# Optimization experiments

Measured on AMD Instinct MI355X. Metric: run time of the kernel, lower is better.

The kernel has to match this reference:

```python
import jax, jax.numpy as jnp
import numpy as np
from jax import lax

A = 3          # anchors per scale
C = 80         # num foreground classes (COCO)
NMS_THRESH = 0.45
NMS_TOPK = 400
POST_NMS = 100


def setup_inputs() -> dict:
    key = jax.random.key(0)
    k0, k1, k2 = jax.random.split(key, 3)
    B = 8
    ch = A * (C + 5)  # 255
    # raw head outputs (pre-decode conv activations), modest scale so exp() stays sane
    tip0 = jax.random.normal(k0, (B, ch, 19, 19), jnp.float32) * 0.5
    tip1 = jax.random.normal(k1, (B, ch, 38, 38), jnp.float32) * 0.5
    tip2 = jax.random.normal(k2, (B, ch, 76, 76), jnp.float32) * 0.5
    # standard YOLOv3 COCO anchors, deepest scale (stride 32) first
    anchors0 = jnp.array([[116., 90.], [156., 198.], [373., 326.]], jnp.float32)
    anchors1 = jnp.array([[30., 61.], [62., 45.], [59., 119.]], jnp.float32)
    anchors2 = jnp.array([[10., 13.], [16., 30.], [33., 23.]], jnp.float32)
    return dict(tip0=tip0, tip1=tip1, tip2=tip2,
                anchors0=anchors0, anchors1=anchors1, anchors2=anchors2)


def _decode(tip, anchors, stride):
    """YOLOOutputV3 inference decode. tip: (B, A*(C+5), H, W)."""
    B, _, H, W = tip.shape
    # (B, A*(C+5), H*W) -> (B, H*W, A, C+5)
    pred = tip.reshape(B, A * (C + 5), H * W).transpose(0, 2, 1).reshape(B, H * W, A, C + 5)
    gx, gy = jnp.meshgrid(jnp.arange(W), jnp.arange(H))       # each (H, W)
    offsets = jnp.stack([gx, gy], -1).reshape(1, H * W, 1, 2).astype(tip.dtype)
    centers = (jax.nn.sigmoid(pred[..., :2]) + offsets) * stride          # (B,HW,A,2)
    scales = jnp.exp(pred[..., 2:4]) * anchors.reshape(1, 1, A, 2)        # (B,HW,A,2)
    conf = jax.nn.sigmoid(pred[..., 4:5])                                 # objectness
    cls_scores = jax.nn.sigmoid(pred[..., 5:]) * conf                      # (B,HW,A,C)
    wh = scales * 0.5
    bbox = jnp.concatenate([centers - wh, centers + wh], -1)               # corner format
    return bbox.reshape(B, H * W * A, 4), cls_scores.reshape(B, H * W * A, C)


def _pairwise_iou(b):
    """b: (K,4) corner boxes -> (K,K) IoU."""
    x1, y1, x2, y2 = b[:, 0], b[:, 1], b[:, 2], b[:, 3]
    area = jnp.maximum(x2 - x1, 0.) * jnp.maximum(y2 - y1, 0.)
    iw = jnp.maximum(jnp.minimum(x2[:, None], x2[None, :]) - jnp.maximum(x1[:, None], x1[None, :]), 0.)
    ih = jnp.maximum(jnp.minimum(y2[:, None], y2[None, :]) - jnp.maximum(y1[:, None], y1[None, :]), 0.)
    inter = iw * ih
    return inter / (area[:, None] + area[None, :] - inter + 1e-12)


def _nms_single(det):
    """Class-aware greedy NMS on one image. det: (M,6) = (cid, score, x1,y1,x2,y2)."""
    K = NMS_TOPK
    _, idx = lax.top_k(det[:, 1], K)     # sort by score, keep top K
    d = det[idx]                          # (K,6), descending score
    iou = _pairwise_iou(d[:, 2:6])
    same = d[:, 0][:, None] == d[:, 0][None, :]   # only same class suppresses
    valid = d[:, 1] > 0.
    rng = jnp.arange(K)

    def body(i, keep):
        sup = (iou[i] > NMS_THRESH) & same[i] & (rng > i) & keep[i] & valid[i]
        return keep & ~sup

    keep = lax.fori_loop(0, K, body, jnp.ones((K,), bool)) & valid
    d = jnp.where(keep[:, None], d, jnp.full_like(d, -1.))
    order = jnp.argsort(-d[:, 1])         # kept (sorted) first, suppressed (-1) last
    return d[order][:POST_NMS]            # (POST_NMS, 6)


def _detect(tip0, tip1, tip2, anchors0, anchors1, anchors2):
    dets = []
    for tip, anc, stride in ((tip0, anchors0, 32), (tip1, anchors1, 16), (tip2, anchors2, 8)):
        bbox, scores = _decode(tip, anc, stride)          # (B,N,4), (B,N,C)
        B, N, _ = bbox.shape
        ids = jnp.broadcast_to(jnp.arange(C, dtype=bbox.dtype)[None, None, :, None], (B, N, C, 1))
        sc = scores[..., None]                            # (B,N,C,1)
        bx = jnp.broadcast_to(bbox[:, :, None, :], (B, N, C, 4))
        dets.append(jnp.concatenate([ids, sc, bx], -1).reshape(B, N * C, 6))
    det = jnp.concatenate(dets, 1)                        # (B, M, 6)
    return jax.vmap(_nms_single)(det)                     # (B, POST_NMS, 6)


def reference(tip0, tip1, tip2, anchors0, anchors1, anchors2):
    res = _detect(tip0, tip1, tip2, anchors0, anchors1, anchors2)
    ids = res[..., 0:1]
    scores = res[..., 1:2]
    bboxes = res[..., 2:6]
    return ids, scores, bboxes
```

## Files before the change

### kernel.cpp

```cpp
#include <hip/hip_runtime.h>
#include <stdint.h>

#define NUMA 3
#define NUMC 80
#define CAP  49152
#define CAP2 8192
#define KTOP 400
#define POST 100
#define NBIN1 2048
#define EQCAP 1024
#define KEY0 0x3EE66666u
#define LBUF 1024
#define NMASK (KTOP * 7)

typedef float f32x4 __attribute__((ext_vector_type(4)));

__device__ __forceinline__ float sigmoidf_(float x) { return 1.0f / (1.0f + expf(-x)); }
__device__ __forceinline__ unsigned uminu(unsigned a, unsigned b) { return a < b ? a : b; }

__global__ void init_kernel(unsigned* __restrict__ p) {
    int i = blockIdx.x * blockDim.x + threadIdx.x;
    if (i < NBIN1 * 16 + 40) p[i] = 0;
}

__global__ __launch_bounds__(256) void score_main(
        const float* __restrict__ t0, const float* __restrict__ t1,
        const float* __restrict__ t2,
        unsigned* __restrict__ ccnt, unsigned* __restrict__ ckey,
        unsigned* __restrict__ cidx)
{
    __shared__ unsigned lkey[LBUF], lidx[LBUF];
    __shared__ unsigned lcnt, lbase;
    const int tid = threadIdx.x;
    if (tid == 0) lcnt = 0;
    __syncthreads();

    const int ba = blockIdx.z;
    const int b = ba / 3, a = ba - 3 * b;
    const int c0 = blockIdx.y * 8;
    const int cx = blockIdx.x;

    #define LEMIT(SC, IDX) do { \
        unsigned key_ = __float_as_uint(SC); \
        if (key_ >= KEY0) { \
            unsigned pos_ = atomicAdd(&lcnt, 1u); \
            if (pos_ < LBUF) { lkey[pos_] = key_; lidx[pos_] = (IDX); } \
        } \
    } while (0)

    if (cx < 2) {
        const int hw = cx * 256 + tid;
        if (hw < 361) {
            const float* base = t0 + (size_t)(b * 255 + a * 85) * 361;
            float cr = base[4 * 361 + hw];
            const float* p0 = base + (size_t)(5 + c0) * 361 + hw;
            float x0 = p0[0 * 361], x1 = p0[1 * 361], x2 = p0[2 * 361], x3 = p0[3 * 361];
            float x4 = p0[4 * 361], x5 = p0[5 * 361], x6 = p0[6 * 361], x7 = p0[7 * 361];
            float cf = sigmoidf_(cr);
            unsigned ib = (unsigned)((hw * NUMA + a) * NUMC + c0);
            LEMIT(sigmoidf_(x0) * cf, ib + 0);
            LEMIT(sigmoidf_(x1) * cf, ib + 1);
            LEMIT(sigmoidf_(x2) * cf, ib + 2);
            LEMIT(sigmoidf_(x3) * cf, ib + 3);
            LEMIT(sigmoidf_(x4) * cf, ib + 4);
            LEMIT(sigmoidf_(x5) * cf, ib + 5);
            LEMIT(sigmoidf_(x6) * cf, ib + 6);
            LEMIT(sigmoidf_(x7) * cf, ib + 7);
        }
    } else {
        const float* tip; int vHW, v, candOff;
        if (cx < 4) { tip = t1; vHW = 361;  v = (cx - 2) * 256 + tid; candOff = 86640; }
        else        { tip = t2; vHW = 1444; v = (cx - 4) * 256 + tid; candOff = 433200; }
        if (v < vHW) {
            const f32x4* bp = (const f32x4*)(tip + (size_t)(b * 255 + a * 85) * (size_t)(vHW * 4));
            f32x4 cv = bp[(size_t)4 * vHW + v];
            const f32x4* p0 = bp + (size_t)(5 + c0) * vHW + v;
            f32x4 s0 = p0[0 * (size_t)vHW], s1 = p0[1 * (size_t)vHW];
            f32x4 s2 = p0[2 * (size_t)vHW], s3 = p0[3 * (size_t)vHW];
            f32x4 s4 = p0[4 * (size_t)vHW], s5 = p0[5 * (size_t)vHW];
            f32x4 s6 = p0[6 * (size_t)vHW], s7 = p0[7 * (size_t)vHW];
            float cf0 = sigmoidf_(cv[0]), cf1 = sigmoidf_(cv[1]);
            float cf2 = sigmoidf_(cv[2]), cf3 = sigmoidf_(cv[3]);
            unsigned ib0 = (unsigned)(candOff + (v * 4 * NUMA + a) * NUMC + c0);
            #define EMIT4(S, U) do { \
                unsigned ib = ib0 + (U); \
                LEMIT(sigmoidf_((S)[0]) * cf0, ib); \
                LEMIT(sigmoidf_((S)[1]) * cf1, ib + 240); \
                LEMIT(sigmoidf_((S)[2]) * cf2, ib + 480); \
                LEMIT(sigmoidf_((S)[3]) * cf3, ib + 720); \
            } while (0)
            EMIT4(s0, 0); EMIT4(s1, 1); EMIT4(s2, 2); EMIT4(s3, 3);
            EMIT4(s4, 4); EMIT4(s5, 5); EMIT4(s6, 6); EMIT4(s7, 7);
            #undef EMIT4
        }
    }
    #undef LEMIT

    __syncthreads();
    if (tid == 0) {
        unsigned c = lcnt;
        if (c > LBUF) {
            atomicOr(&ccnt[b], 0x80000000u);
            lbase = 0xFFFFFFFFu;
        } else {
            lbase = atomicAdd(&ccnt[b], c);
        }
    }
    __syncthreads();
    unsigned c = uminu(lcnt, (unsigned)LBUF);
    unsigned basep = lbase;
    if (basep != 0xFFFFFFFFu) {
        for (unsigned i = tid; i < c; i += 256) {
            unsigned p = basep + i;
            if (p < CAP) {
                ckey[(size_t)b * CAP + p] = lkey[i];
                cidx[(size_t)b * CAP + p] = lidx[i];
            }
        }
    }
}

__device__ __forceinline__ void wave_select(const unsigned* h, int nbins, unsigned rank,
                                            unsigned* resv, int tid)
{
    if (tid >= 64) return;
    const int lane = tid;
    const int cs = nbins >> 6;
    unsigned v = 0;
    for (int k = 0; k < cs; k++) {
        int off = (k + lane) & (cs - 1);
        v += h[lane * cs + off];
    }
    unsigned S = v;
    #pragma unroll
    for (int o = 1; o < 64; o <<= 1) {
        unsigned t = (unsigned)__shfl_down((int)S, o);
        if (lane + o < 64) S += t;
    }
    unsigned long long bm = __ballot(S >= rank);
    if (bm == 0ull) bm = 1ull;
    int C = 63 - __builtin_clzll(bm);
    unsigned SC = (unsigned)__builtin_amdgcn_readlane((int)S, C);
    unsigned vC = (unsigned)__builtin_amdgcn_readlane((int)v, C);
    unsigned rem = rank - (SC - vC);
    unsigned w = (lane < cs) ? h[C * cs + lane] : 0u;
    unsigned T = w;
    #pragma unroll
    for (int o = 1; o < 64; o <<= 1) {
        unsigned t = (unsigned)__shfl_down((int)T, o);
        if (lane + o < 64) T += t;
    }
    unsigned long long bm2 = __ballot((T >= rem) && (lane < cs));
    if (bm2 == 0ull) bm2 = 1ull;
    int B = 63 - __builtin_clzll(bm2);
    unsigned TB = (unsigned)__builtin_amdgcn_readlane((int)T, B);
    unsigned wB = (unsigned)__builtin_amdgcn_readlane((int)w, B);
    if (lane == 0) {
        resv[0] = (unsigned)(C * cs + B);
        resv[1] = rem - (TB - wB);
    }
}

__global__ __launch_bounds__(1024) void findcut_v(const unsigned* __restrict__ ckey,
                                                  unsigned* __restrict__ cutfloor,
                                                  unsigned* __restrict__ ccnt,
                                                  unsigned* __restrict__ flags) {
    __shared__ unsigned h[NBIN1];
    __shared__ unsigned resv[2];
    int b = blockIdx.x;
    int tid = threadIdx.x;
    for (int i = tid; i < NBIN1; i += 1024) h[i] = 0;
    unsigned c = ccnt[b];
    bool ok = (c >= KTOP) && (c <= CAP);
    __syncthreads();
    if (ok) {
        const unsigned* ck = ckey + (size_t)b * CAP;
        for (unsigned i = tid; i < c; i += 1024) {
            unsigned bin = (ck[i] - KEY0) >> 13;
            atomicAdd(&h[uminu(bin, NBIN1 - 1)], 1u);
        }
    }
    __syncthreads();
    wave_select(h, NBIN1, KTOP, resv, tid);
    __syncthreads();
    if (tid == 0) {
        flags[b] = ok ? 1u : 0u;
        if (ok) {
            cutfloor[b] = KEY0 + (resv[0] << 13);
        } else {
            cutfloor[b] = 0u;
            ccnt[b] = 0;
        }
    }
}

__global__ __launch_bounds__(256) void fb_hist(
        const float* __restrict__ t0, const float* __restrict__ t1,
        const float* __restrict__ t2,
        unsigned* __restrict__ histF, const unsigned* __restrict__ flags)
{
    const int ba = blockIdx.z;
    const int b = ba / 3, a = ba - 3 * b;
    if (flags[b]) return;
    __shared__ unsigned lh[NBIN1];
    const int tid = threadIdx.x;
    for (int i = tid; i < NBIN1; i += 256) lh[i] = 0;
    __syncthreads();
    const int c0 = blockIdx.y * 8;
    const int cx = blockIdx.x;
    if (cx < 2) {
        const int hw = cx * 256 + tid;
        if (hw < 361) {
            const float* base = t0 + (size_t)(b * 255 + a * 85) * 361;
            float cf = sigmoidf_(base[4 * 361 + hw]);
            for (int u = 0; u < 8; u++) {
                float sc = sigmoidf_(base[(size_t)(5 + c0 + u) * 361 + hw]) * cf;
                atomicAdd(&lh[__float_as_uint(sc) >> 19], 1u);
            }
        }
    } else {
        const float* tip; int vHW, v;
        if (cx < 4) { tip = t1; vHW = 361;  v = (cx - 2) * 256 + tid; }
        else        { tip = t2; vHW = 1444; v = (cx - 4) * 256 + tid; }
        if (v < vHW) {
            const f32x4* bp = (const f32x4*)(tip + (size_t)(b * 255 + a * 85) * (size_t)(vHW * 4));
            f32x4 cv = bp[(size_t)4 * vHW + v];
            float cf[4] = { sigmoidf_(cv[0]), sigmoidf_(cv[1]), sigmoidf_(cv[2]), sigmoidf_(cv[3]) };
            for (int u = 0; u < 8; u++) {
                f32x4 s = bp[(size_t)(5 + c0 + u) * vHW + v];
                for (int l = 0; l < 4; l++)
                    atomicAdd(&lh[__float_as_uint(sigmoidf_(s[l]) * cf[l]) >> 19], 1u);
            }
        }
    }
    __syncthreads();
    unsigned* gh = histF + b * NBIN1;
    for (int i = tid; i < NBIN1; i += 256) {
        unsigned v2 = lh[i];
        if (v2) atomicAdd(&gh[i], v2);
    }
}

__global__ __launch_bounds__(256) void fb_cut(const unsigned* __restrict__ histF,
                                              unsigned* __restrict__ cutb,
                                              const unsigned* __restrict__ flags) {
    int b = blockIdx.x;
    if (flags[b]) return;
    __shared__ unsigned h[NBIN1];
    __shared__ unsigned resv[2];
    for (int i = threadIdx.x; i < NBIN1; i += 256) h[i] = histF[b * NBIN1 + i];
    __syncthreads();
    wave_select(h, NBIN1, KTOP, resv, threadIdx.x);
    __syncthreads();
    if (threadIdx.x == 0) cutb[b] = resv[0];
}

__global__ __launch_bounds__(256) void fb_compact(
        const float* __restrict__ t0, const float* __restrict__ t1,
        const float* __restrict__ t2,
        const unsigned* __restrict__ cutb, unsigned* __restrict__ ccnt,
        unsigned* __restrict__ ckey, unsigned* __restrict__ cidx,
        const unsigned* __restrict__ flags)
{
    const int ba = blockIdx.z;
    const int b = ba / 3, a = ba - 3 * b;
    if (flags[b]) return;
    const int tid = threadIdx.x;
    const int c0 = blockIdx.y * 8;
    const int cx = blockIdx.x;
    unsigned cutkey = cutb[b] << 19;

    if (cx < 2) {
        const int hw = cx * 256 + tid;
        if (hw < 361) {
            const float* base = t0 + (size_t)(b * 255 + a * 85) * 361;
            float cf = sigmoidf_(base[4 * 361 + hw]);
            for (int u = 0; u < 8; u++) {
                float sc = sigmoidf_(base[(size_t)(5 + c0 + u) * 361 + hw]) * cf;
                unsigned key = __float_as_uint(sc);
                if (key >= cutkey) {
                    unsigned pos = atomicAdd(&ccnt[b], 1u);
                    if (pos < CAP) {
                        ckey[(size_t)b * CAP + pos] = key;
                        cidx[(size_t)b * CAP + pos] = (unsigned)((hw * NUMA + a) * NUMC + c0 + u);
                    }
                }
            }
        }
    } else {
        const float* tip; int vHW, v, candOff;
        if (cx < 4) { tip = t1; vHW = 361;  v = (cx - 2) * 256 + tid; candOff = 86640; }
        else        { tip = t2; vHW = 1444; v = (cx - 4) * 256 + tid; candOff = 433200; }
        if (v < vHW) {
            const f32x4* bp = (const f32x4*)(tip + (size_t)(b * 255 + a * 85) * (size_t)(vHW * 4));
            f32x4 cv = bp[(size_t)4 * vHW + v];
            float cf[4] = { sigmoidf_(cv[0]), sigmoidf_(cv[1]), sigmoidf_(cv[2]), sigmoidf_(cv[3]) };
            unsigned ib0 = (unsigned)(candOff + (v * 4 * NUMA + a) * NUMC + c0);
            for (int u = 0; u < 8; u++) {
                f32x4 s = bp[(size_t)(5 + c0 + u) * vHW + v];
                for (int l = 0; l < 4; l++) {
                    float sc = sigmoidf_(s[l]) * cf[l];
                    unsigned key = __float_as_uint(sc);
                    if (key >= cutkey) {
                        unsigned pos = atomicAdd(&ccnt[b], 1u);
                        if (pos < CAP) {
                            ckey[(size_t)b * CAP + pos] = key;
                            cidx[(size_t)b * CAP + pos] = ib0 + (unsigned)u + (unsigned)l * 240;
                        }
                    }
                }
            }
        }
    }
}

__global__ __launch_bounds__(256) void prefilter(
        const unsigned* __restrict__ ckey, const unsigned* __restrict__ cidx,
        const unsigned* __restrict__ ccnt, const unsigned* __restrict__ cutfloor,
        unsigned* __restrict__ cnt2, unsigned* __restrict__ ckey2,
        unsigned* __restrict__ cidx2)
{
    __shared__ unsigned lk[2048], li[2048];
    __shared__ unsigned lcnt, lbase;
    const int tid = threadIdx.x;
    const int b = blockIdx.z;
    if (tid == 0) lcnt = 0;
    __syncthreads();
    const unsigned n = uminu(ccnt[b], (unsigned)CAP);
    const unsigned cutf = cutfloor[b];
    const unsigned* ck = ckey + (size_t)b * CAP;
    const unsigned* ci = cidx + (size_t)b * CAP;
    for (unsigned i = blockIdx.x * 256 + tid; i < n; i += 32 * 256) {
        unsigned k = ck[i];
        if (k >= cutf) {
            unsigned p = atomicAdd(&lcnt, 1u);
            if (p < 2048u) { lk[p] = k; li[p] = ci[i]; }
        }
    }
    __syncthreads();
    if (tid == 0) lbase = atomicAdd(&cnt2[b], uminu(lcnt, 2048u));
    __syncthreads();
    unsigned c = uminu(lcnt, 2048u);
    for (unsigned i = tid; i < c; i += 256) {
        unsigned p = lbase + i;
        if (p < CAP2) {
            ckey2[(size_t)b * CAP2 + p] = lk[i];
            cidx2[(size_t)b * CAP2 + p] = li[i];
        }
    }
}

__global__ __launch_bounds__(512) void topk_kernel(
        const float* __restrict__ t0, const float* __restrict__ t1,
        const float* __restrict__ t2,
        const float* __restrict__ anc0, const float* __restrict__ anc1,
        const float* __restrict__ anc2,
        const unsigned* __restrict__ ckey, const unsigned* __restrict__ cidx,
        const unsigned* __restrict__ ccnt,
        const unsigned* __restrict__ ckey2, const unsigned* __restrict__ cidx2,
        const unsigned* __restrict__ cnt2,
        float* __restrict__ dX1, float* __restrict__ dY1,
        float* __restrict__ dX2, float* __restrict__ dY2,
        float* __restrict__ dSC, unsigned* __restrict__ dCID)
{
    const int b = blockIdx.x;
    const int tid = threadIdx.x;
    const int T = 512;

    __shared__ unsigned hist[4096];
    __shared__ unsigned resv[2];
    __shared__ unsigned selk[512], seli[512];
    __shared__ unsigned eqi[EQCAP];
    __shared__ unsigned cnts[2];

    unsigned n2 = cnt2[b];
    const unsigned* ck; const unsigned* ci; unsigned n;
    if (n2 <= (unsigned)CAP2) {
        ck = ckey2 + (size_t)b * CAP2; ci = cidx2 + (size_t)b * CAP2; n = n2;
    } else {
        ck = ckey + (size_t)b * CAP; ci = cidx + (size_t)b * CAP;
        n = uminu(ccnt[b], (unsigned)CAP);
    }

    for (int i = tid; i < NBIN1; i += T) hist[i] = 0;
    __syncthreads();
    for (unsigned i = tid; i < n; i += T) atomicAdd(&hist[ck[i] >> 19], 1u);
    __syncthreads();
    wave_select(hist, NBIN1, KTOP, resv, tid);
    __syncthreads();
    unsigned b1 = resv[0], r2 = resv[1];
    __syncthreads();

    for (int i = tid; i < 4096; i += T) hist[i] = 0;
    __syncthreads();
    for (unsigned i = tid; i < n; i += T) {
        unsigned k = ck[i];
        if ((k >> 19) == b1) atomicAdd(&hist[(k >> 7) & 0xFFFu], 1u);
    }
    __syncthreads();
    wave_select(hist, 4096, r2, resv, tid);
    __syncthreads();
    unsigned b2 = resv[0], r3 = resv[1];
    __syncthreads();

    for (int i = tid; i < 128; i += T) hist[i] = 0;
    __syncthreads();
    unsigned pref = (b1 << 12) | b2;
    for (unsigned i = tid; i < n; i += T) {
        unsigned k = ck[i];
        if ((k >> 7) == pref) atomicAdd(&hist[k & 127u], 1u);
    }
    __syncthreads();
    wave_select(hist, 128, r3, resv, tid);
    __syncthreads();
    unsigned b3 = resv[0], needEq = resv[1];
    unsigned K400 = (b1 << 19) | (b2 << 7) | b3;
    __syncthreads();

    selk[tid] = 0u; seli[tid] = 0xFFFFFFFFu;
    for (int i = tid; i < EQCAP; i += T) eqi[i] = 0xFFFFFFFFu;
    if (tid == 0) { cnts[0] = 0; cnts[1] = 0; }
    __syncthreads();
    for (unsigned i = tid; i < n; i += T) {
        unsigned k = ck[i];
        if (k > K400) {
            unsigned p = atomicAdd(&cnts[0], 1u);
            if (p < KTOP) { selk[p] = k; seli[p] = ci[i]; }
        } else if (k == K400) {
            unsigned q = atomicAdd(&cnts[1], 1u);
            if (q < EQCAP) eqi[q] = ci[i];
        }
    }
    __syncthreads();
    unsigned selCnt = uminu(cnts[0], (unsigned)KTOP);
    unsigned eqN   = uminu(cnts[1], (unsigned)EQCAP);

    if (eqN > needEq) {
        int P2 = 1; while ((unsigned)P2 < eqN) P2 <<= 1;
        for (int k2 = 2; k2 <= P2; k2 <<= 1) {
            for (int j = k2 >> 1; j > 0; j >>= 1) {
                __syncthreads();
                for (int i = tid; i < P2; i += T) {
                    int ixj = i ^ j;
                    if (ixj > i && ixj < P2) {
                        unsigned va = eqi[i], vb = eqi[ixj];
                        bool up = ((i & k2) == 0);
                        if (up ? (va > vb) : (va < vb)) { eqi[i] = vb; eqi[ixj] = va; }
                    }
                }
            }
        }
        __syncthreads();
    }
    for (unsigned t2v = tid; t2v < needEq; t2v += T) {
        unsigned p = selCnt + t2v;
        if (p < KTOP) { selk[p] = K400; seli[p] = eqi[t2v]; }
    }
    __syncthreads();

    for (int k2 = 2; k2 <= 512; k2 <<= 1) {
        int j = k2 >> 1;
        for (; j >= 64; j >>= 1) {
            __syncthreads();
            int i = tid, ixj = i ^ j;
            if (ixj > i) {
                unsigned ka = selk[i], kb = selk[ixj], ia = seli[i], ib = seli[ixj];
                bool before = (ka > kb) || (ka == kb && ia < ib);
                bool up = ((i & k2) == 0);
                if (up ? !before : before) {
                    selk[i] = kb; selk[ixj] = ka; seli[i] = ib; seli[ixj] = ia;
                }
            }
        }
        __syncthreads();
        for (; j > 0; j >>= 1) {
            int i = tid, ixj = i ^ j;
            if (ixj > i) {
                unsigned ka = selk[i], kb = selk[ixj], ia = seli[i], ib = seli[ixj];
                bool before = (ka > kb) || (ka == kb && ia < ib);
                bool up = ((i & k2) == 0);
                if (up ? !before : before) {
                    selk[i] = kb; selk[ixj] = ka; seli[i] = ib; seli[ixj] = ia;
                }
            }
        }
    }
    __syncthreads();

    if (tid < KTOP) {
        unsigned idx = seli[tid];
        const float* tip; const float* anc; int HW, W, candOff; float strideF;
        if (idx < 86640u)       { tip = t0; anc = anc0; HW = 361;  W = 19; strideF = 32.f; candOff = 0; }
        else if (idx < 433200u) { tip = t1; anc = anc1; HW = 1444; W = 38; strideF = 16.f; candOff = 86640; }
        else                    { tip = t2; anc = anc2; HW = 5776; W = 76; strideF = 8.f;  candOff = 433200; }
        unsigned local = idx - (unsigned)candOff;
        int cls = (int)(local % NUMC);
        int nn  = (int)(local / NUMC);
        int a = nn % NUMA, hwl = nn / NUMA;
        const float* base = tip + (size_t)(b * 255 + a * 85) * HW + hwl;
        float tx = base[0];
        float ty = base[(size_t)HW];
        float tw = base[(size_t)2 * HW];
        float th = base[(size_t)3 * HW];
        float fx = (float)(hwl % W), fy = (float)(hwl / W);
        float cx = (sigmoidf_(tx) + fx) * strideF;
        float cy = (sigmoidf_(ty) + fy) * strideF;
        float hw_ = expf(tw) * anc[2 * a]     * 0.5f;
        float hh_ = expf(th) * anc[2 * a + 1] * 0.5f;
        int o = b * KTOP + tid;
        dX1[o] = cx - hw_; dY1[o] = cy - hh_;
        dX2[o] = cx + hw_; dY2[o] = cy + hh_;
        dSC[o] = __uint_as_float(selk[tid]);
        dCID[o] = (unsigned)cls;
    }
}

__global__ __launch_bounds__(256) void mask_kernel(
        const float* __restrict__ dX1, const float* __restrict__ dY1,
        const float* __restrict__ dX2, const float* __restrict__ dY2,
        const unsigned* __restrict__ dCID, unsigned long long* __restrict__ maskG)
{
    __shared__ float lx1[KTOP], ly1[KTOP], lx2[KTOP], ly2[KTOP];
    __shared__ int lcid[KTOP];
    const int b = blockIdx.y;
    const int tid = threadIdx.x;
    for (int i = tid; i < KTOP; i += 256) {
        int o = b * KTOP + i;
        lx1[i] = dX1[o]; ly1[i] = dY1[o];
        lx2[i] = dX2[o]; ly2[i] = dY2[o];
        lcid[i] = (int)dCID[o];
    }
    __syncthreads();
    int p = blockIdx.x * 256 + tid;
    if (p < NMASK) {
        int i = p / 7, w = p - i * 7;
        float x1i = lx1[i], y1i = ly1[i], x2i = lx2[i], y2i = ly2[i];
        float ai = fmaxf(x2i - x1i, 0.f) * fmaxf(y2i - y1i, 0.f);
        int cidI = lcid[i];
        unsigned long long m = 0ull;
        int j0 = w * 64;
        int j1 = j0 + 64; if (j1 > KTOP) j1 = KTOP;
        int js = j0 > i + 1 ? j0 : i + 1;
        for (int j = js; j < j1; j++) {
            if (lcid[j] != cidI) continue;
            float iw = fminf(x2i, lx2[j]) - fmaxf(x1i, lx1[j]);
            float ih = fminf(y2i, ly2[j]) - fmaxf(y1i, ly1[j]);
            iw = fmaxf(iw, 0.f); ih = fmaxf(ih, 0.f);
            float inter = iw * ih;
            float aj = fmaxf(lx2[j] - lx1[j], 0.f) * fmaxf(ly2[j] - ly1[j], 0.f);
            float iou = inter / (ai + aj - inter + 1e-12f);
            if (iou > 0.45f) m |= (1ull << (j - j0));
        }
        maskG[(size_t)b * NMASK + p] = m;
    }
}

__global__ __launch_bounds__(512) void greedy_kernel(
        const float* __restrict__ dX1, const float* __restrict__ dY1,
        const float* __restrict__ dX2, const float* __restrict__ dY2,
        const float* __restrict__ dSC, const unsigned* __restrict__ dCID,
        const unsigned long long* __restrict__ maskG, float* __restrict__ out)
{
    __shared__ unsigned long long maskL[NMASK];
    __shared__ unsigned long long vkeep[7];
    __shared__ float oid[POST], osc[POST], obb[POST * 4];
    const int b = blockIdx.x;
    const int tid = threadIdx.x;

    for (int i = tid; i < NMASK; i += 512) maskL[i] = maskG[(size_t)b * NMASK + i];
    if (tid < POST) { oid[tid] = -1.f; osc[tid] = -1.f; }
    if (tid < POST * 4) obb[tid] = -1.f;
    __syncthreads();

    if (tid < 64) {
        const int lane = tid;
        unsigned long long keep = 0ull;
        if (lane < 7) keep = (lane == 6) ? 0xFFFFull : ~0ull;
        unsigned long long mb[8];
        #pragma unroll
        for (int k = 0; k < 8; k++)
            mb[k] = (lane < 7) ? maskL[k * 7 + lane] : 0ull;
        for (int ib = 0; ib < KTOP; ib += 8) {
            #pragma unroll
            for (int k = 0; k < 8; k++) {
                int i = ib + k;
                unsigned long long m = mb[k];
                int nf = ib + 8 + k;
                mb[k] = (lane < 7 && nf < KTOP) ? maskL[nf * 7 + lane] : 0ull;
                int w = i >> 6;
                unsigned klo = (unsigned)__builtin_amdgcn_readlane((int)(unsigned)(keep & 0xFFFFFFFFull), w);
                unsigned khi = (unsigned)__builtin_amdgcn_readlane((int)(unsigned)(keep >> 32), w);
                unsigned long long kw = ((unsigned long long)khi << 32) | klo;
                if ((kw >> (i & 63)) & 1ull) keep &= ~m;
            }
        }
        if (lane < 7) vkeep[lane] = keep;
    }
    __syncthreads();

    if (tid < KTOP) {
        int w = tid >> 6, bp = tid & 63;
        unsigned long long kw = vkeep[w];
        if ((kw >> bp) & 1ull) {
            int r = 0;
            for (int q = 0; q < w; q++) r += __popcll(vkeep[q]);
            r += __popcll(kw & ((1ull << bp) - 1ull));
            if (r < POST) {
                int o = b * KTOP + tid;
                oid[r] = (float)(int)dCID[o];
                osc[r] = dSC[o];
                obb[r * 4 + 0] = dX1[o];
                obb[r * 4 + 1] = dY1[o];
                obb[r * 4 + 2] = dX2[o];
                obb[r * 4 + 3] = dY2[o];
            }
        }
    }
    __syncthreads();
    if (tid < POST) {
        out[b * POST + tid]       = oid[tid];
        out[800 + b * POST + tid] = osc[tid];
    }
    if (tid < POST * 4) out[1600 + b * POST * 4 + tid] = obb[tid];
}

extern "C" void kernel_launch(void* const* d_in, const int* in_sizes, int n_in,
                              void* d_out, int out_size, void* d_ws, size_t ws_size,
                              hipStream_t stream)
{
    const float* tip0 = (const float*)d_in[0];
    const float* tip1 = (const float*)d_in[1];
    const float* tip2 = (const float*)d_in[2];
    const float* anc0 = (const float*)d_in[3];
    const float* anc1 = (const float*)d_in[4];
    const float* anc2 = (const float*)d_in[5];
    float* out = (float*)d_out;

    unsigned* histN    = (unsigned*)d_ws;
    unsigned* histF    = histN + 8 * NBIN1;
    unsigned* cutb     = histF + 8 * NBIN1;
    unsigned* cutfloor = cutb + 8;
    unsigned* ccnt     = cutfloor + 8;
    unsigned* cnt2     = ccnt + 8;
    unsigned* flags    = cnt2 + 8;
    unsigned* ckey     = flags + 8;
    unsigned* cidx     = ckey + (size_t)8 * CAP;
    unsigned* ckey2    = cidx + (size_t)8 * CAP;
    unsigned* cidx2    = ckey2 + (size_t)8 * CAP2;
    float*    dX1      = (float*)(cidx2 + (size_t)8 * CAP2);
    float*    dY1      = dX1 + 8 * KTOP;
    float*    dX2      = dY1 + 8 * KTOP;
    float*    dY2      = dX2 + 8 * KTOP;
    float*    dSC      = dY2 + 8 * KTOP;
    unsigned* dCID     = (unsigned*)(dSC + 8 * KTOP);
    unsigned long long* maskG = (unsigned long long*)(dCID + 8 * KTOP);

    init_kernel<<<(NBIN1 * 16 + 40 + 255) / 256, 256, 0, stream>>>(histN);

    dim3 g(10, 10, 24);
    score_main<<<g, 256, 0, stream>>>(tip0, tip1, tip2, ccnt, ckey, cidx);
    findcut_v<<<8, 1024, 0, stream>>>(ckey, cutfloor, ccnt, flags);
    fb_hist<<<g, 256, 0, stream>>>(tip0, tip1, tip2, histF, flags);
    fb_cut<<<8, 256, 0, stream>>>(histF, cutb, flags);
    fb_compact<<<g, 256, 0, stream>>>(tip0, tip1, tip2, cutb, ccnt, ckey, cidx, flags);
    prefilter<<<dim3(32, 1, 8), 256, 0, stream>>>(ckey, cidx, ccnt, cutfloor,
                                                  cnt2, ckey2, cidx2);
    topk_kernel<<<8, 512, 0, stream>>>(tip0, tip1, tip2, anc0, anc1, anc2,
                                       ckey, cidx, ccnt, ckey2, cidx2, cnt2,
                                       dX1, dY1, dX2, dY2, dSC, dCID);
    mask_kernel<<<dim3((NMASK + 255) / 256, 8), 256, 0, stream>>>(
        dX1, dY1, dX2, dY2, dCID, maskG);
    greedy_kernel<<<8, 512, 0, stream>>>(dX1, dY1, dX2, dY2, dSC, dCID, maskG, out);
}
```

Baseline: 204.1 us.

## Fuse top-k, IoU mask and greedy NMS into one kernel; drop cut and prefilter passes

The separate findcut and prefilter kernels are removed, so top-k reads the compacted candidate list directly. Top-k, pairwise IoU mask construction and greedy suppression are merged into one per-image kernel that keeps boxes and masks in shared memory instead of round-tripping through global memory. The score grid now handles 10 classes per block instead of 8, giving fewer blocks. This cuts the launch count from ten to six and drops the intermediate global buffers. In exchange, top-k may scan the full candidate list without prefiltering, and the mask build runs on only 8 blocks, which limits parallelism.

```diff
diff --git a/kernel.cpp b/kernel.cpp
--- a/kernel.cpp
+++ b/kernel.cpp
@@ -4,7 +4,6 @@
 #define NUMA 3
 #define NUMC 80
 #define CAP  49152
-#define CAP2 8192
 #define KTOP 400
 #define POST 100
 #define NBIN1 2048
@@ -20,7 +19,7 @@
 
 __global__ void init_kernel(unsigned* __restrict__ p) {
     int i = blockIdx.x * blockDim.x + threadIdx.x;
-    if (i < NBIN1 * 16 + 40) p[i] = 0;
+    if (i < NBIN1 * 8 + 40) p[i] = 0;
 }
 
 __global__ __launch_bounds__(256) void score_main(
@@ -37,7 +36,7 @@
 
     const int ba = blockIdx.z;
     const int b = ba / 3, a = ba - 3 * b;
-    const int c0 = blockIdx.y * 8;
+    const int c0 = blockIdx.y * 10;
     const int cx = blockIdx.x;
 
     #define LEMIT(SC, IDX) do { \
@@ -56,6 +55,7 @@
             const float* p0 = base + (size_t)(5 + c0) * 361 + hw;
             float x0 = p0[0 * 361], x1 = p0[1 * 361], x2 = p0[2 * 361], x3 = p0[3 * 361];
             float x4 = p0[4 * 361], x5 = p0[5 * 361], x6 = p0[6 * 361], x7 = p0[7 * 361];
+            float x8 = p0[8 * 361], x9 = p0[9 * 361];
             float cf = sigmoidf_(cr);
             unsigned ib = (unsigned)((hw * NUMA + a) * NUMC + c0);
             LEMIT(sigmoidf_(x0) * cf, ib + 0);
@@ -66,6 +66,8 @@
             LEMIT(sigmoidf_(x5) * cf, ib + 5);
             LEMIT(sigmoidf_(x6) * cf, ib + 6);
             LEMIT(sigmoidf_(x7) * cf, ib + 7);
+            LEMIT(sigmoidf_(x8) * cf, ib + 8);
+            LEMIT(sigmoidf_(x9) * cf, ib + 9);
         }
     } else {
         const float* tip; int vHW, v, candOff;
@@ -79,6 +81,7 @@
             f32x4 s2 = p0[2 * (size_t)vHW], s3 = p0[3 * (size_t)vHW];
             f32x4 s4 = p0[4 * (size_t)vHW], s5 = p0[5 * (size_t)vHW];
             f32x4 s6 = p0[6 * (size_t)vHW], s7 = p0[7 * (size_t)vHW];
+            f32x4 s8 = p0[8 * (size_t)vHW], s9 = p0[9 * (size_t)vHW];
             float cf0 = sigmoidf_(cv[0]), cf1 = sigmoidf_(cv[1]);
             float cf2 = sigmoidf_(cv[2]), cf3 = sigmoidf_(cv[3]);
             unsigned ib0 = (unsigned)(candOff + (v * 4 * NUMA + a) * NUMC + c0);
@@ -91,6 +94,7 @@
             } while (0)
             EMIT4(s0, 0); EMIT4(s1, 1); EMIT4(s2, 2); EMIT4(s3, 3);
             EMIT4(s4, 4); EMIT4(s5, 5); EMIT4(s6, 6); EMIT4(s7, 7);
+            EMIT4(s8, 8); EMIT4(s9, 9);
             #undef EMIT4
         }
     }
@@ -161,59 +165,27 @@
     }
 }
 
-__global__ __launch_bounds__(1024) void findcut_v(const unsigned* __restrict__ ckey,
-                                                  unsigned* __restrict__ cutfloor,
-                                                  unsigned* __restrict__ ccnt,
-                                                  unsigned* __restrict__ flags) {
-    __shared__ unsigned h[NBIN1];
-    __shared__ unsigned resv[2];
-    int b = blockIdx.x;
-    int tid = threadIdx.x;
-    for (int i = tid; i < NBIN1; i += 1024) h[i] = 0;
-    unsigned c = ccnt[b];
-    bool ok = (c >= KTOP) && (c <= CAP);
-    __syncthreads();
-    if (ok) {
-        const unsigned* ck = ckey + (size_t)b * CAP;
-        for (unsigned i = tid; i < c; i += 1024) {
-            unsigned bin = (ck[i] - KEY0) >> 13;
-            atomicAdd(&h[uminu(bin, NBIN1 - 1)], 1u);
-        }
-    }
-    __syncthreads();
-    wave_select(h, NBIN1, KTOP, resv, tid);
-    __syncthreads();
-    if (tid == 0) {
-        flags[b] = ok ? 1u : 0u;
-        if (ok) {
-            cutfloor[b] = KEY0 + (resv[0] << 13);
-        } else {
-            cutfloor[b] = 0u;
-            ccnt[b] = 0;
-        }
-    }
-}
-
 __global__ __launch_bounds__(256) void fb_hist(
         const float* __restrict__ t0, const float* __restrict__ t1,
         const float* __restrict__ t2,
-        unsigned* __restrict__ histF, const unsigned* __restrict__ flags)
+        unsigned* __restrict__ histF, const unsigned* __restrict__ ccnt)
 {
     const int ba = blockIdx.z;
     const int b = ba / 3, a = ba - 3 * b;
-    if (flags[b]) return;
+    unsigned cc = ccnt[b];
+    if (cc >= KTOP && cc <= CAP) return;
     __shared__ unsigned lh[NBIN1];
     const int tid = threadIdx.x;
     for (int i = tid; i < NBIN1; i += 256) lh[i] = 0;
     __syncthreads();
-    const int c0 = blockIdx.y * 8;
+    const int c0 = blockIdx.y * 10;
     const int cx = blockIdx.x;
     if (cx < 2) {
         const int hw = cx * 256 + tid;
         if (hw < 361) {
             const float* base = t0 + (size_t)(b * 255 + a * 85) * 361;
             float cf = sigmoidf_(base[4 * 361 + hw]);
-            for (int u = 0; u < 8; u++) {
+            for (int u = 0; u < 10; u++) {
                 float sc = sigmoidf_(base[(size_t)(5 + c0 + u) * 361 + hw]) * cf;
                 atomicAdd(&lh[__float_as_uint(sc) >> 19], 1u);
             }
@@ -226,7 +198,7 @@
             const f32x4* bp = (const f32x4*)(tip + (size_t)(b * 255 + a * 85) * (size_t)(vHW * 4));
             f32x4 cv = bp[(size_t)4 * vHW + v];
             float cf[4] = { sigmoidf_(cv[0]), sigmoidf_(cv[1]), sigmoidf_(cv[2]), sigmoidf_(cv[3]) };
-            for (int u = 0; u < 8; u++) {
+            for (int u = 0; u < 10; u++) {
                 f32x4 s = bp[(size_t)(5 + c0 + u) * vHW + v];
                 for (int l = 0; l < 4; l++)
                     atomicAdd(&lh[__float_as_uint(sigmoidf_(s[l]) * cf[l]) >> 19], 1u);
@@ -243,30 +215,31 @@
 
 __global__ __launch_bounds__(256) void fb_cut(const unsigned* __restrict__ histF,
                                               unsigned* __restrict__ cutb,
-                                              const unsigned* __restrict__ flags) {
+                                              unsigned* __restrict__ ccnt) {
     int b = blockIdx.x;
-    if (flags[b]) return;
+    unsigned cc = ccnt[b];
+    if (cc >= KTOP && cc <= CAP) return;
     __shared__ unsigned h[NBIN1];
     __shared__ unsigned resv[2];
     for (int i = threadIdx.x; i < NBIN1; i += 256) h[i] = histF[b * NBIN1 + i];
     __syncthreads();
     wave_select(h, NBIN1, KTOP, resv, threadIdx.x);
     __syncthreads();
-    if (threadIdx.x == 0) cutb[b] = resv[0];
+    if (threadIdx.x == 0) { cutb[b] = resv[0]; ccnt[b] = 0; }
 }
 
 __global__ __launch_bounds__(256) void fb_compact(
         const float* __restrict__ t0, const float* __restrict__ t1,
         const float* __restrict__ t2,
         const unsigned* __restrict__ cutb, unsigned* __restrict__ ccnt,
-        unsigned* __restrict__ ckey, unsigned* __restrict__ cidx,
-        const unsigned* __restrict__ flags)
+        unsigned* __restrict__ ckey, unsigned* __restrict__ cidx)
 {
     const int ba = blockIdx.z;
     const int b = ba / 3, a = ba - 3 * b;
-    if (flags[b]) return;
+    unsigned cc = ccnt[b];
+    if (cc >= KTOP && cc <= CAP) return;
     const int tid = threadIdx.x;
-    const int c0 = blockIdx.y * 8;
+    const int c0 = blockIdx.y * 10;
     const int cx = blockIdx.x;
     unsigned cutkey = cutb[b] << 19;
 
@@ -275,7 +248,7 @@
         if (hw < 361) {
             const float* base = t0 + (size_t)(b * 255 + a * 85) * 361;
             float cf = sigmoidf_(base[4 * 361 + hw]);
-            for (int u = 0; u < 8; u++) {
+            for (int u = 0; u < 10; u++) {
                 float sc = sigmoidf_(base[(size_t)(5 + c0 + u) * 361 + hw]) * cf;
                 unsigned key = __float_as_uint(sc);
                 if (key >= cutkey) {
@@ -296,7 +269,7 @@
             f32x4 cv = bp[(size_t)4 * vHW + v];
             float cf[4] = { sigmoidf_(cv[0]), sigmoidf_(cv[1]), sigmoidf_(cv[2]), sigmoidf_(cv[3]) };
             unsigned ib0 = (unsigned)(candOff + (v * 4 * NUMA + a) * NUMC + c0);
-            for (int u = 0; u < 8; u++) {
+            for (int u = 0; u < 10; u++) {
                 f32x4 s = bp[(size_t)(5 + c0 + u) * vHW + v];
                 for (int l = 0; l < 4; l++) {
                     float sc = sigmoidf_(s[l]) * cf[l];
@@ -314,54 +287,13 @@
     }
 }
 
-__global__ __launch_bounds__(256) void prefilter(
-        const unsigned* __restrict__ ckey, const unsigned* __restrict__ cidx,
-        const unsigned* __restrict__ ccnt, const unsigned* __restrict__ cutfloor,
-        unsigned* __restrict__ cnt2, unsigned* __restrict__ ckey2,
-        unsigned* __restrict__ cidx2)
-{
-    __shared__ unsigned lk[2048], li[2048];
-    __shared__ unsigned lcnt, lbase;
-    const int tid = threadIdx.x;
-    const int b = blockIdx.z;
-    if (tid == 0) lcnt = 0;
-    __syncthreads();
-    const unsigned n = uminu(ccnt[b], (unsigned)CAP);
-    const unsigned cutf = cutfloor[b];
-    const unsigned* ck = ckey + (size_t)b * CAP;
-    const unsigned* ci = cidx + (size_t)b * CAP;
-    for (unsigned i = blockIdx.x * 256 + tid; i < n; i += 32 * 256) {
-        unsigned k = ck[i];
-        if (k >= cutf) {
-            unsigned p = atomicAdd(&lcnt, 1u);
-            if (p < 2048u) { lk[p] = k; li[p] = ci[i]; }
-        }
-    }
-    __syncthreads();
-    if (tid == 0) lbase = atomicAdd(&cnt2[b], uminu(lcnt, 2048u));
-    __syncthreads();
-    unsigned c = uminu(lcnt, 2048u);
-    for (unsigned i = tid; i < c; i += 256) {
-        unsigned p = lbase + i;
-        if (p < CAP2) {
-            ckey2[(size_t)b * CAP2 + p] = lk[i];
-            cidx2[(size_t)b * CAP2 + p] = li[i];
-        }
-    }
-}
-
-__global__ __launch_bounds__(512) void topk_kernel(
+__global__ __launch_bounds__(512) void topk_nms(
         const float* __restrict__ t0, const float* __restrict__ t1,
         const float* __restrict__ t2,
         const float* __restrict__ anc0, const float* __restrict__ anc1,
         const float* __restrict__ anc2,
         const unsigned* __restrict__ ckey, const unsigned* __restrict__ cidx,
-        const unsigned* __restrict__ ccnt,
-        const unsigned* __restrict__ ckey2, const unsigned* __restrict__ cidx2,
-        const unsigned* __restrict__ cnt2,
-        float* __restrict__ dX1, float* __restrict__ dY1,
-        float* __restrict__ dX2, float* __restrict__ dY2,
-        float* __restrict__ dSC, unsigned* __restrict__ dCID)
+        const unsigned* __restrict__ ccnt, float* __restrict__ out)
 {
     const int b = blockIdx.x;
     const int tid = threadIdx.x;
@@ -372,15 +304,15 @@
     __shared__ unsigned selk[512], seli[512];
     __shared__ unsigned eqi[EQCAP];
     __shared__ unsigned cnts[2];
-
-    unsigned n2 = cnt2[b];
-    const unsigned* ck; const unsigned* ci; unsigned n;
-    if (n2 <= (unsigned)CAP2) {
-        ck = ckey2 + (size_t)b * CAP2; ci = cidx2 + (size_t)b * CAP2; n = n2;
-    } else {
-        ck = ckey + (size_t)b * CAP; ci = cidx + (size_t)b * CAP;
-        n = uminu(ccnt[b], (unsigned)CAP);
-    }
+    __shared__ float bx1[KTOP], by1[KTOP], bx2[KTOP], by2[KTOP];
+    __shared__ int   bcid[KTOP];
+    __shared__ unsigned long long maskL[NMASK];
+    __shared__ unsigned long long vkeep[7];
+    __shared__ float oid[POST], osc[POST], obb[POST * 4];
+
+    const unsigned* ck = ckey + (size_t)b * CAP;
+    const unsigned* ci = cidx + (size_t)b * CAP;
+    unsigned n = uminu(ccnt[b], (unsigned)CAP);
 
     for (int i = tid; i < NBIN1; i += T) hist[i] = 0;
     __syncthreads();
@@ -507,69 +439,35 @@
         float cy = (sigmoidf_(ty) + fy) * strideF;
         float hw_ = expf(tw) * anc[2 * a]     * 0.5f;
         float hh_ = expf(th) * anc[2 * a + 1] * 0.5f;
-        int o = b * KTOP + tid;
-        dX1[o] = cx - hw_; dY1[o] = cy - hh_;
-        dX2[o] = cx + hw_; dY2[o] = cy + hh_;
-        dSC[o] = __uint_as_float(selk[tid]);
-        dCID[o] = (unsigned)cls;
-    }
-}
-
-__global__ __launch_bounds__(256) void mask_kernel(
-        const float* __restrict__ dX1, const float* __restrict__ dY1,
-        const float* __restrict__ dX2, const float* __restrict__ dY2,
-        const unsigned* __restrict__ dCID, unsigned long long* __restrict__ maskG)
-{
-    __shared__ float lx1[KTOP], ly1[KTOP], lx2[KTOP], ly2[KTOP];
-    __shared__ int lcid[KTOP];
-    const int b = blockIdx.y;
-    const int tid = threadIdx.x;
-    for (int i = tid; i < KTOP; i += 256) {
-        int o = b * KTOP + i;
-        lx1[i] = dX1[o]; ly1[i] = dY1[o];
-        lx2[i] = dX2[o]; ly2[i] = dY2[o];
-        lcid[i] = (int)dCID[o];
-    }
-    __syncthreads();
-    int p = blockIdx.x * 256 + tid;
-    if (p < NMASK) {
+        bx1[tid] = cx - hw_; by1[tid] = cy - hh_;
+        bx2[tid] = cx + hw_; by2[tid] = cy + hh_;
+        bcid[tid] = cls;
+    }
+    if (tid < POST) { oid[tid] = -1.f; osc[tid] = -1.f; }
+    if (tid < POST * 4) obb[tid] = -1.f;
+    __syncthreads();
+
+    for (int p = tid; p < NMASK; p += T) {
         int i = p / 7, w = p - i * 7;
-        float x1i = lx1[i], y1i = ly1[i], x2i = lx2[i], y2i = ly2[i];
+        float x1i = bx1[i], y1i = by1[i], x2i = bx2[i], y2i = by2[i];
         float ai = fmaxf(x2i - x1i, 0.f) * fmaxf(y2i - y1i, 0.f);
-        int cidI = lcid[i];
+        int cidI = bcid[i];
         unsigned long long m = 0ull;
         int j0 = w * 64;
         int j1 = j0 + 64; if (j1 > KTOP) j1 = KTOP;
         int js = j0 > i + 1 ? j0 : i + 1;
         for (int j = js; j < j1; j++) {
-            if (lcid[j] != cidI) continue;
-            float iw = fminf(x2i, lx2[j]) - fmaxf(x1i, lx1[j]);
-            float ih = fminf(y2i, ly2[j]) - fmaxf(y1i, ly1[j]);
+            if (bcid[j] != cidI) continue;
+            float iw = fminf(x2i, bx2[j]) - fmaxf(x1i, bx1[j]);
+            float ih = fminf(y2i, by2[j]) - fmaxf(y1i, by1[j]);
             iw = fmaxf(iw, 0.f); ih = fmaxf(ih, 0.f);
             float inter = iw * ih;
-            float aj = fmaxf(lx2[j] - lx1[j], 0.f) * fmaxf(ly2[j] - ly1[j], 0.f);
+            float aj = fmaxf(bx2[j] - bx1[j], 0.f) * fmaxf(by2[j] - by1[j], 0.f);
             float iou = inter / (ai + aj - inter + 1e-12f);
             if (iou > 0.45f) m |= (1ull << (j - j0));
         }
-        maskG[(size_t)b * NMASK + p] = m;
-    }
-}
-
-__global__ __launch_bounds__(512) void greedy_kernel(
-        const float* __restrict__ dX1, const float* __restrict__ dY1,
-        const float* __restrict__ dX2, const float* __restrict__ dY2,
-        const float* __restrict__ dSC, const unsigned* __restrict__ dCID,
-        const unsigned long long* __restrict__ maskG, float* __restrict__ out)
-{
-    __shared__ unsigned long long maskL[NMASK];
-    __shared__ unsigned long long vkeep[7];
-    __shared__ float oid[POST], osc[POST], obb[POST * 4];
-    const int b = blockIdx.x;
-    const int tid = threadIdx.x;
-
-    for (int i = tid; i < NMASK; i += 512) maskL[i] = maskG[(size_t)b * NMASK + i];
-    if (tid < POST) { oid[tid] = -1.f; osc[tid] = -1.f; }
-    if (tid < POST * 4) obb[tid] = -1.f;
+        maskL[p] = m;
+    }
     __syncthreads();
 
     if (tid < 64) {
@@ -606,13 +504,12 @@
             for (int q = 0; q < w; q++) r += __popcll(vkeep[q]);
             r += __popcll(kw & ((1ull << bp) - 1ull));
             if (r < POST) {
-                int o = b * KTOP + tid;
-                oid[r] = (float)(int)dCID[o];
-                osc[r] = dSC[o];
-                obb[r * 4 + 0] = dX1[o];
-                obb[r * 4 + 1] = dY1[o];
-                obb[r * 4 + 2] = dX2[o];
-                obb[r * 4 + 3] = dY2[o];
+                oid[r] = (float)bcid[tid];
+                osc[r] = __uint_as_float(selk[tid]);
+                obb[r * 4 + 0] = bx1[tid];
+                obb[r * 4 + 1] = by1[tid];
+                obb[r * 4 + 2] = bx2[tid];
+                obb[r * 4 + 3] = by2[tid];
             }
         }
     }
@@ -645,30 +542,15 @@
     unsigned* flags    = cnt2 + 8;
     unsigned* ckey     = flags + 8;
     unsigned* cidx     = ckey + (size_t)8 * CAP;
-    unsigned* ckey2    = cidx + (size_t)8 * CAP;
-    unsigned* cidx2    = ckey2 + (size_t)8 * CAP2;
-    float*    dX1      = (float*)(cidx2 + (size_t)8 * CAP2);
-    float*    dY1      = dX1 + 8 * KTOP;
-    float*    dX2      = dY1 + 8 * KTOP;
-    float*    dY2      = dX2 + 8 * KTOP;
-    float*    dSC      = dY2 + 8 * KTOP;
-    unsigned* dCID     = (unsigned*)(dSC + 8 * KTOP);
-    unsigned long long* maskG = (unsigned long long*)(dCID + 8 * KTOP);
-
-    init_kernel<<<(NBIN1 * 16 + 40 + 255) / 256, 256, 0, stream>>>(histN);
-
-    dim3 g(10, 10, 24);
+    (void)histN; (void)cnt2; (void)flags;
+
+    init_kernel<<<(NBIN1 * 8 + 40 + 255) / 256, 256, 0, stream>>>(histF);
+
+    dim3 g(10, 8, 24);
     score_main<<<g, 256, 0, stream>>>(tip0, tip1, tip2, ccnt, ckey, cidx);
-    findcut_v<<<8, 1024, 0, stream>>>(ckey, cutfloor, ccnt, flags);
-    fb_hist<<<g, 256, 0, stream>>>(tip0, tip1, tip2, histF, flags);
-    fb_cut<<<8, 256, 0, stream>>>(histF, cutb, flags);
-    fb_compact<<<g, 256, 0, stream>>>(tip0, tip1, tip2, cutb, ccnt, ckey, cidx, flags);
-    prefilter<<<dim3(32, 1, 8), 256, 0, stream>>>(ckey, cidx, ccnt, cutfloor,
-                                                  cnt2, ckey2, cidx2);
-    topk_kernel<<<8, 512, 0, stream>>>(tip0, tip1, tip2, anc0, anc1, anc2,
-                                       ckey, cidx, ccnt, ckey2, cidx2, cnt2,
-                                       dX1, dY1, dX2, dY2, dSC, dCID);
-    mask_kernel<<<dim3((NMASK + 255) / 256, 8), 256, 0, stream>>>(
-        dX1, dY1, dX2, dY2, dCID, maskG);
-    greedy_kernel<<<8, 512, 0, stream>>>(dX1, dY1, dX2, dY2, dSC, dCID, maskG, out);
-}
+    fb_hist<<<g, 256, 0, stream>>>(tip0, tip1, tip2, histF, ccnt);
+    fb_cut<<<8, 256, 0, stream>>>(histF, cutb, ccnt);
+    fb_compact<<<g, 256, 0, stream>>>(tip0, tip1, tip2, cutb, ccnt, ckey, cidx);
+    topk_nms<<<8, 512, 0, stream>>>(tip0, tip1, tip2, anc0, anc1, anc2,
+                                    ckey, cidx, ccnt, out);
+}
```

Result: slower. 251.6 us (+23.3%).
